# Kernel tuning notes

Measured on AMD Instinct MI355X. Metric: run time of the kernel, lower is better.

The kernel has to match this reference:

```python
import jax, jax.numpy as jnp
import numpy as np

BN_EPS = 1e-5


def _bn_train(x, gamma, beta):
    # torch BatchNorm1d in training mode: normalize with batch mean and
    # biased batch variance.
    mu = jnp.mean(x, axis=0)
    var = jnp.var(x, axis=0)
    return (x - mu) * jax.lax.rsqrt(var + BN_EPS) * gamma + beta


def setup_inputs() -> dict:
    key = jax.random.key(0)
    ks = jax.random.split(key, 12)
    N, F_D, F_C, E, VOCAB, H = 16384, 26, 10, 16, 200000, 400
    D_IN = (F_D + F_C) * E  # 576
    return {
        "Xi_dense": jax.random.normal(ks[0], (N, F_D, 1), jnp.float32),
        "Xv": jax.random.uniform(ks[1], (N, F_D + F_C), jnp.float32),
        "Wd": jax.random.normal(ks[2], (F_D, E), jnp.float32) * 0.1,
        "bd": jax.random.normal(ks[3], (F_D, E), jnp.float32) * 0.1,
        "tables": jax.random.normal(ks[4], (F_C, VOCAB, E), jnp.float32) * 0.1,
        "W1": jax.random.normal(ks[5], (H, D_IN), jnp.float32) * 0.05,
        "b1": jax.random.normal(ks[6], (H,), jnp.float32) * 0.05,
        "g1": jnp.ones((H,), jnp.float32),
        "be1": jnp.zeros((H,), jnp.float32),
        "W2": jax.random.normal(ks[7], (H, H), jnp.float32) * 0.05,
        "b2": jax.random.normal(ks[8], (H,), jnp.float32) * 0.05,
        "g2": jnp.ones((H,), jnp.float32),
        "be2": jnp.zeros((H,), jnp.float32),
        "bias_vec": jax.random.normal(ks[9], (N,), jnp.float32),
        "Xi_cat": jax.random.randint(ks[10], (N, F_C, 1), 0, VOCAB, jnp.int32),
    }


def reference(Xi_dense, Xv, Wd, bd, tables, W1, b1, g1, be1,
              W2, b2, g2, be2, bias_vec, Xi_cat):
    N = Xi_dense.shape[0]
    # dense fields: per-field Linear(1, E) -> x * W + b, shape (N, 26, E)
    dense_emb = Xi_dense * Wd[None] + bd[None]  # (N,26,1)*(1,26,E) broadcast
    # categorical fields: per-field embedding lookup, shape (N, 10, E)
    cat_emb = jax.vmap(lambda tbl, idx: tbl[idx], in_axes=(0, 1), out_axes=1)(
        tables, Xi_cat[:, :, 0])
    # scale each field embedding by its Xv value
    all_emb = jnp.concatenate([dense_emb, cat_emb], axis=1) * Xv[:, :, None]  # (N,36,E)

    # fm first order: concat of all scaled field embeddings
    fm_first = all_emb.reshape(N, -1)  # (N, 576)
    # fm second order: 0.5 * ((sum)^2 - sum of squares)
    s = jnp.sum(all_emb, axis=1)                       # (N, E)
    fm_second = 0.5 * (s * s - jnp.sum(all_emb * all_emb, axis=1))  # (N, E)

    # deep part: Linear -> BatchNorm (train-mode stats) per hidden layer;
    # dropout p=0 -> identity.
    deep = fm_first
    deep = _bn_train(deep @ W1.T + b1, g1, be1)
    deep = _bn_train(deep @ W2.T + b2, g2, be2)

    total = (jnp.sum(fm_first, axis=1) + jnp.sum(fm_second, axis=1)
             + jnp.sum(deep, axis=1) + bias_vec)
    return total
```

## Files before the change

kernel.cpp:

```cpp
#include <hip/hip_runtime.h>

#define BN_EPS 1e-5f

typedef unsigned short u16;
typedef __attribute__((ext_vector_type(8))) short bf16x8;
typedef __attribute__((ext_vector_type(4))) float f32x4;

__device__ __forceinline__ u16 f2bf(float x) {
  union { float f; unsigned int u; } v; v.f = x;
  unsigned int r = v.u + 0x7fffu + ((v.u >> 16) & 1u);
  return (u16)(r >> 16);
}
__device__ __forceinline__ float bf2f(u16 h) {
  union { unsigned int u; float f; } v; v.u = ((unsigned int)h) << 16;
  return v.f;
}

__device__ __forceinline__ float wave_reduce_sum(float v) {
#pragma unroll
  for (int off = 1; off < 64; off <<= 1) v += __shfl_xor(v, off, 64);
  return v;
}

__device__ __forceinline__ void gload_lds16(const void* g, void* l) {
  __builtin_amdgcn_global_load_lds(
      (const __attribute__((address_space(1))) void*)g,
      (__attribute__((address_space(3))) void*)l, 16, 0, 0);
}

__global__ __launch_bounds__(256) void embed_prep(
    const float* __restrict__ Xi_dense, const float* __restrict__ Xv,
    const float* __restrict__ Wd, const float* __restrict__ bd,
    const float* __restrict__ tables, const int* __restrict__ Xi_cat,
    const float* __restrict__ bias_vec, const float* __restrict__ W1,
    u16* __restrict__ fm_first, float* __restrict__ partial,
    u16* __restrict__ W1h, float* __restrict__ statz) {
  const int t = threadIdx.x;
  if (blockIdx.x >= 256) {
    const int bb = blockIdx.x - 256;
    if (bb == 0) {
#pragma unroll
      for (int i = 0; i < 8; ++i) statz[i * 256 + t] = 0.f;
    }
    const int base = bb * 4096;
#pragma unroll
    for (int e = 0; e < 16; ++e) {
      const int idx = base + e * 256 + t;
      const int r = idx / 576;
      const int j = idx - r * 576;
      W1h[idx] = (r < 400) ? f2bf(W1[r * 576 + j]) : (u16)0;
    }
    return;
  }

  __shared__ float Xvs[64 * 37];
  __shared__ float Xds[64 * 27];
  __shared__ int Cis[64 * 11];
  __shared__ float Wds[416], Bds[416];
  const int n0 = blockIdx.x * 64;

  for (int i = t; i < 2304; i += 256) {
    const int r = i / 36;
    Xvs[r * 37 + (i - r * 36)] = Xv[n0 * 36 + i];
  }
  for (int i = t; i < 1664; i += 256) {
    const int r = i / 26;
    Xds[r * 27 + (i - r * 26)] = Xi_dense[n0 * 26 + i];
  }
  for (int i = t; i < 640; i += 256) {
    const int r = i / 10;
    Cis[r * 11 + (i - r * 10)] = Xi_cat[n0 * 10 + i];
  }
  for (int i = t; i < 416; i += 256) {
    Wds[i] = Wd[i];
    Bds[i] = bd[i];
  }
  __syncthreads();

  const int r = t >> 2, q = t & 3;
  const int n = n0 + r;
  const int fpar = q >> 1, eh = (q & 1) * 8;
  float s8[8] = {}, q8[8] = {};
  float sum_all = 0.f;
  u16* frow = fm_first + (size_t)n * 576;

#pragma unroll
  for (int k = 0; k < 18; ++k) {
    const int f = fpar + 2 * k;
    const float xvv = Xvs[r * 37 + f];
    float val[8];
    if (k < 13) {
      const float xd = Xds[r * 27 + f];
      const float4 w0 = *(const float4*)&Wds[f * 16 + eh];
      const float4 w1 = *(const float4*)&Wds[f * 16 + eh + 4];
      const float4 b0 = *(const float4*)&Bds[f * 16 + eh];
      const float4 b1 = *(const float4*)&Bds[f * 16 + eh + 4];
      val[0] = fmaf(xd, w0.x, b0.x) * xvv;
      val[1] = fmaf(xd, w0.y, b0.y) * xvv;
      val[2] = fmaf(xd, w0.z, b0.z) * xvv;
      val[3] = fmaf(xd, w0.w, b0.w) * xvv;
      val[4] = fmaf(xd, w1.x, b1.x) * xvv;
      val[5] = fmaf(xd, w1.y, b1.y) * xvv;
      val[6] = fmaf(xd, w1.z, b1.z) * xvv;
      val[7] = fmaf(xd, w1.w, b1.w) * xvv;
    } else {
      const int fc = f - 26;
      const int row = Cis[r * 11 + fc];
      const float* tp =
          tables + ((size_t)fc * 200000 + (size_t)row) * 16 + eh;
      const float4 v0 = *(const float4*)tp;
      const float4 v1 = *(const float4*)(tp + 4);
      val[0] = v0.x * xvv;
      val[1] = v0.y * xvv;
      val[2] = v0.z * xvv;
      val[3] = v0.w * xvv;
      val[4] = v1.x * xvv;
      val[5] = v1.y * xvv;
      val[6] = v1.z * xvv;
      val[7] = v1.w * xvv;
    }
    bf16x8 o;
#pragma unroll
    for (int j = 0; j < 8; ++j) {
      s8[j] += val[j];
      q8[j] += val[j] * val[j];
      sum_all += val[j];
      o[j] = (short)f2bf(val[j]);
    }
    *(bf16x8*)&frow[f * 16 + eh] = o;
  }

  float fm2h = 0.f;
#pragma unroll
  for (int j = 0; j < 8; ++j) {
    const float se = s8[j] + __shfl_xor(s8[j], 2, 64);
    const float qe = q8[j] + __shfl_xor(q8[j], 2, 64);
    fm2h += se * se - qe;
  }
  const float fm2 = 0.5f * (fm2h + __shfl_xor(fm2h, 1, 64));
  float srow = sum_all + __shfl_xor(sum_all, 1, 64);
  srow += __shfl_xor(srow, 2, 64);
  if (q == 0) partial[n] = srow + fm2 + bias_vec[n];
}

template <int NFR>
__device__ __forceinline__ void gemm_body(
    const u16* __restrict__ A, int lda, const u16* __restrict__ W, int ldw,
    const float* __restrict__ bias, int nbias, u16* __restrict__ Y, int ldc,
    int Ncap, float* __restrict__ aS, float* __restrict__ aQ, int K,
    int bx, int by, u16* As, u16* Bs, float (&rS)[2][4][2][16],
    float (&rQ)[2][4][2][16]) {
  const int t = threadIdx.x;
  const int bm = bx * 64;
  const int bn = by * 128;
  const int wid = t >> 6, lane = t & 63;
  const int wr = wid >> 1, wc = wid & 1;
  const int lr = lane & 15, lk = (lane >> 4) * 8;
  const int sr = lane >> 2;
  const int sk = (lane & 3) * 8;
  const bool active = (NFR == 4) || (wc == 0);

  f32x4 acc[2][NFR] = {};

  for (int kt = 0; kt < K; kt += 32) {
    gload_lds16(&A[(size_t)(bm + wid * 16 + sr) * lda + kt + sk],
                &As[wid * 512]);
#pragma unroll
    for (int i = 0; i < 2; ++i) {
      const int c = wid * 2 + i;
      if (NFR == 4 || c < 2)
        gload_lds16(&W[(size_t)(bn + c * 16 + sr) * ldw + kt + sk],
                    &Bs[c * 512]);
    }
    __syncthreads();

    if (active) {
      bf16x8 af[2], bfv[NFR];
#pragma unroll
      for (int mf = 0; mf < 2; ++mf)
        af[mf] = *(const bf16x8*)&As[(wr * 32 + mf * 16 + lr) * 32 + lk];
#pragma unroll
      for (int nf = 0; nf < NFR; ++nf)
        bfv[nf] = *(const bf16x8*)&Bs[(wc * 64 + nf * 16 + lr) * 32 + lk];
#pragma unroll
      for (int mf = 0; mf < 2; ++mf)
#pragma unroll
        for (int nf = 0; nf < NFR; ++nf)
          acc[mf][nf] = __builtin_amdgcn_mfma_f32_16x16x32_bf16(
              af[mf], bfv[nf], acc[mf][nf], 0, 0, 0);
    }
    __syncthreads();
  }

  const int l4 = (lane >> 4) * 4;
  if (active) {
#pragma unroll
    for (int nf = 0; nf < NFR; ++nf) {
      const int col = bn + wc * 64 + nf * 16 + lr;
      const float bb = (col < nbias) ? bias[col] : 0.f;
      float s = 0.f, q = 0.f;
#pragma unroll
      for (int mf = 0; mf < 2; ++mf) {
#pragma unroll
        for (int r = 0; r < 4; ++r) {
          const int row = bm + wr * 32 + mf * 16 + l4 + r;
          const float v = acc[mf][nf][r] + bb;
          s += v;
          q += v * v;
          if (col < Ncap) Y[(size_t)row * ldc + col] = f2bf(v);
        }
      }
      s += __shfl_xor(s, 16, 64);
      s += __shfl_xor(s, 32, 64);
      q += __shfl_xor(q, 16, 64);
      q += __shfl_xor(q, 32, 64);
      if (lane < 16) {
        rS[wc][nf][wr][lr] = s;
        rQ[wc][nf][wr][lr] = q;
      }
    }
  }
  __syncthreads();
  if (t < (NFR == 4 ? 128 : 32)) {
    const int wcc = t >> 6, nff = (t >> 4) & 3, c = t & 15;
    atomicAdd(&aS[bn + t], rS[wcc][nff][0][c] + rS[wcc][nff][1][c]);
    atomicAdd(&aQ[bn + t], rQ[wcc][nff][0][c] + rQ[wcc][nff][1][c]);
  }
}

__global__ __launch_bounds__(256) void gemm_bf16(
    const u16* __restrict__ A, int lda,
    const u16* __restrict__ W, int ldw,
    const float* __restrict__ bias, int nbias,
    u16* __restrict__ Y, int ldc, int Ncap,
    float* __restrict__ aS, float* __restrict__ aQ, int K) {
  __shared__ u16 As[64 * 32];
  __shared__ u16 Bs[128 * 32];
  __shared__ float rS[2][4][2][16];
  __shared__ float rQ[2][4][2][16];
  const int bid = blockIdx.x;
  const int l = (bid & 7) * (gridDim.x >> 3) + (bid >> 3);
  const int bx = l >> 2, by = l & 3;
  if (by < 3)
    gemm_body<4>(A, lda, W, ldw, bias, nbias, Y, ldc, Ncap, aS, aQ, K,
                 bx, by, As, Bs, rS, rQ);
  else
    gemm_body<2>(A, lda, W, ldw, bias, nbias, Y, ldc, Ncap, aS, aQ, K,
                 bx, by, As, Bs, rS, rQ);
}

__device__ __forceinline__ void bn_affine4(const float* aS, const float* aQ,
                                           const float* g, const float* be,
                                           int j, float4& aa, float4& cc) {
  const float4 S = *(const float4*)&aS[j];
  const float4 Q = *(const float4*)&aQ[j];
  const float4 G = *(const float4*)&g[j];
  const float4 E = *(const float4*)&be[j];
  const float inv = 1.f / 16384.f;
  float mu, var;
  mu = S.x * inv; var = Q.x * inv - mu * mu;
  aa.x = G.x * rsqrtf(var + BN_EPS); cc.x = E.x - mu * aa.x;
  mu = S.y * inv; var = Q.y * inv - mu * mu;
  aa.y = G.y * rsqrtf(var + BN_EPS); cc.y = E.y - mu * aa.y;
  mu = S.z * inv; var = Q.z * inv - mu * mu;
  aa.z = G.z * rsqrtf(var + BN_EPS); cc.z = E.z - mu * aa.z;
  mu = S.w * inv; var = Q.w * inv - mu * mu;
  aa.w = G.w * rsqrtf(var + BN_EPS); cc.w = E.w - mu * aa.w;
}

__global__ __launch_bounds__(256) void prep2(
    const float* __restrict__ aS1, const float* __restrict__ aQ1,
    const float* __restrict__ g1, const float* __restrict__ be1,
    const float* __restrict__ W2, const float* __restrict__ b2,
    u16* __restrict__ W2p, float* __restrict__ b2p) {
  const int t = threadIdx.x;
  const int lane = t & 63;
  const int row = blockIdx.x * 4 + (t >> 6);
  const ushort4 z4 = {0, 0, 0, 0};
  if (row >= 400) {
    const int j1 = lane * 4;
    *(ushort4*)&W2p[(size_t)row * 416 + j1] = z4;
    const int j2 = 256 + lane * 4;
    if (j2 < 416) *(ushort4*)&W2p[(size_t)row * 416 + j2] = z4;
    if (lane == 0) b2p[row] = 0.f;
    return;
  }
  float dot = 0.f;
  {
    const int j = lane * 4;
    float4 aa, cc;
    bn_affine4(aS1, aQ1, g1, be1, j, aa, cc);
    const float4 w = *(const float4*)&W2[(size_t)row * 400 + j];
    ushort4 o = {f2bf(w.x * aa.x), f2bf(w.y * aa.y), f2bf(w.z * aa.z),
                 f2bf(w.w * aa.w)};
    *(ushort4*)&W2p[(size_t)row * 416 + j] = o;
    dot += w.x * cc.x + w.y * cc.y + w.z * cc.z + w.w * cc.w;
  }
  {
    const int j = 256 + lane * 4;
    if (j < 400) {
      float4 aa, cc;
      bn_affine4(aS1, aQ1, g1, be1, j, aa, cc);
      const float4 w = *(const float4*)&W2[(size_t)row * 400 + j];
      ushort4 o = {f2bf(w.x * aa.x), f2bf(w.y * aa.y), f2bf(w.z * aa.z),
                   f2bf(w.w * aa.w)};
      *(ushort4*)&W2p[(size_t)row * 416 + j] = o;
      dot += w.x * cc.x + w.y * cc.y + w.z * cc.z + w.w * cc.w;
    } else if (j < 416) {
      *(ushort4*)&W2p[(size_t)row * 416 + j] = z4;
    }
  }
  dot = wave_reduce_sum(dot);
  if (lane == 0) b2p[row] = b2[row] + dot;
}

__global__ __launch_bounds__(256) void final_kernel(
    const u16* __restrict__ Y2, const float* __restrict__ aS2,
    const float* __restrict__ aQ2, const float* __restrict__ g2,
    const float* __restrict__ be2, const float* __restrict__ partial,
    float* __restrict__ out) {
  const int t = threadIdx.x;
  const int lane = t & 63;
  const int wid = t >> 6;
  const int j0 = lane * 8;
  float ar[8], cr[8];
  if (j0 < 400) {
    float4 aa0, cc0, aa1, cc1;
    bn_affine4(aS2, aQ2, g2, be2, j0, aa0, cc0);
    bn_affine4(aS2, aQ2, g2, be2, j0 + 4, aa1, cc1);
    ar[0] = aa0.x; ar[1] = aa0.y; ar[2] = aa0.z; ar[3] = aa0.w;
    ar[4] = aa1.x; ar[5] = aa1.y; ar[6] = aa1.z; ar[7] = aa1.w;
    cr[0] = cc0.x; cr[1] = cc0.y; cr[2] = cc0.z; cr[3] = cc0.w;
    cr[4] = cc1.x; cr[5] = cc1.y; cr[6] = cc1.z; cr[7] = cc1.w;
  } else {
#pragma unroll
    for (int k = 0; k < 8; ++k) { ar[k] = 0.f; cr[k] = 0.f; }
  }
#pragma unroll
  for (int r = 0; r < 4; ++r) {
    const int n = blockIdx.x * 16 + wid * 4 + r;
    float acc = 0.f;
    if (j0 < 400) {
      const bf16x8 y = *(const bf16x8*)&Y2[(size_t)n * 400 + j0];
#pragma unroll
      for (int k = 0; k < 8; ++k)
        acc += fmaf(ar[k], bf2f((u16)y[k]), cr[k]);
    }
    acc = wave_reduce_sum(acc);
    if (lane == 0) out[n] = partial[n] + acc;
  }
}

extern "C" void kernel_launch(void* const* d_in, const int* in_sizes, int n_in,
                              void* d_out, int out_size, void* d_ws,
                              size_t ws_size, hipStream_t stream) {
  const float* Xi_dense = (const float*)d_in[0];
  const float* Xv = (const float*)d_in[1];
  const float* Wd = (const float*)d_in[2];
  const float* bd = (const float*)d_in[3];
  const float* tables = (const float*)d_in[4];
  const float* W1 = (const float*)d_in[5];
  const float* b1 = (const float*)d_in[6];
  const float* g1 = (const float*)d_in[7];
  const float* be1 = (const float*)d_in[8];
  const float* W2 = (const float*)d_in[9];
  const float* b2 = (const float*)d_in[10];
  const float* g2 = (const float*)d_in[11];
  const float* be2 = (const float*)d_in[12];
  const float* bias_vec = (const float*)d_in[13];
  const int* Xi_cat = (const int*)d_in[14];

  constexpr int N = 16384;
  constexpr int DIN = 576;
  constexpr int H = 400;
  constexpr int KP = 416;
  constexpr int WPAD = 512;
  constexpr int NXB = 256;

  u16* fm_first = (u16*)d_ws;
  u16* Y1h = fm_first + (size_t)N * DIN;
  u16* Y2h = Y1h + (size_t)N * KP;
  u16* W1h = Y2h + (size_t)N * H;
  u16* W2p = W1h + (size_t)WPAD * DIN;
  float* fptr = (float*)(W2p + (size_t)WPAD * KP);
  float* partial = fptr;
  float* aS1 = partial + N;
  float* aQ1 = aS1 + WPAD;
  float* aS2 = aQ1 + WPAD;
  float* aQ2 = aS2 + WPAD;
  float* b2p = aQ2 + WPAD;

  embed_prep<<<256 + 72, 256, 0, stream>>>(Xi_dense, Xv, Wd, bd, tables,
                                           Xi_cat, bias_vec, W1, fm_first,
                                           partial, W1h, aS1);

  gemm_bf16<<<NXB * 4, 256, 0, stream>>>(fm_first, DIN, W1h, DIN, b1, H,
                                         Y1h, KP, KP, aS1, aQ1, DIN);

  prep2<<<128, 256, 0, stream>>>(aS1, aQ1, g1, be1, W2, b2, W2p, b2p);

  gemm_bf16<<<NXB * 4, 256, 0, stream>>>(Y1h, KP, W2p, KP, b2p, H,
                                         Y2h, H, H, aS2, aQ2, KP);

  final_kernel<<<N / 16, 256, 0, stream>>>(Y2h, aS2, aQ2, g2, be2, partial,
                                           (float*)d_out);
}
```

Measured before the change: 69.79 us.

## Drop linear biases cancelled by train-mode BatchNorm and widen embed parallelism

Train-mode BatchNorm subtracts the batch mean, so any per-column constant added before it cancels. The change therefore removes the b1/b2 bias adds from the GEMM epilogues and drops the folded-bias dot product (and beta1) from prep2, which becomes a simple elementwise weight-scaling kernel. Separately, embed_prep now handles 32 rows per block with 8 threads per row instead of 64 rows with 4 threads, doubling the block count and adding one extra shuffle stage to the reductions. This relies on the algebraic cancellation being exact; bf16 rounding of the unbiased activations changes slightly.

```diff
diff --git a/kernel.cpp b/kernel.cpp
--- a/kernel.cpp
+++ b/kernel.cpp
@@ -36,8 +36,8 @@
     u16* __restrict__ fm_first, float* __restrict__ partial,
     u16* __restrict__ W1h, float* __restrict__ statz) {
   const int t = threadIdx.x;
-  if (blockIdx.x >= 256) {
-    const int bb = blockIdx.x - 256;
+  if (blockIdx.x >= 512) {
+    const int bb = blockIdx.x - 512;
     if (bb == 0) {
 #pragma unroll
       for (int i = 0; i < 8; ++i) statz[i * 256 + t] = 0.f;
@@ -53,21 +53,21 @@
     return;
   }
 
-  __shared__ float Xvs[64 * 37];
-  __shared__ float Xds[64 * 27];
-  __shared__ int Cis[64 * 11];
+  __shared__ float Xvs[32 * 37];
+  __shared__ float Xds[32 * 27];
+  __shared__ int Cis[32 * 11];
   __shared__ float Wds[416], Bds[416];
-  const int n0 = blockIdx.x * 64;
-
-  for (int i = t; i < 2304; i += 256) {
+  const int n0 = blockIdx.x * 32;
+
+  for (int i = t; i < 1152; i += 256) {
     const int r = i / 36;
     Xvs[r * 37 + (i - r * 36)] = Xv[n0 * 36 + i];
   }
-  for (int i = t; i < 1664; i += 256) {
+  for (int i = t; i < 832; i += 256) {
     const int r = i / 26;
     Xds[r * 27 + (i - r * 26)] = Xi_dense[n0 * 26 + i];
   }
-  for (int i = t; i < 640; i += 256) {
+  for (int i = t; i < 320; i += 256) {
     const int r = i / 10;
     Cis[r * 11 + (i - r * 10)] = Xi_cat[n0 * 10 + i];
   }
@@ -77,32 +77,32 @@
   }
   __syncthreads();
 
-  const int r = t >> 2, q = t & 3;
+  const int r = t >> 3, q = t & 7;
   const int n = n0 + r;
-  const int fpar = q >> 1, eh = (q & 1) * 8;
+  const int fbase = q >> 1, eh = (q & 1) * 8;
   float s8[8] = {}, q8[8] = {};
   float sum_all = 0.f;
   u16* frow = fm_first + (size_t)n * 576;
 
 #pragma unroll
-  for (int k = 0; k < 18; ++k) {
-    const int f = fpar + 2 * k;
+  for (int j = 0; j < 9; ++j) {
+    const int f = fbase + 4 * j;
     const float xvv = Xvs[r * 37 + f];
     float val[8];
-    if (k < 13) {
+    if (f < 26) {
       const float xd = Xds[r * 27 + f];
       const float4 w0 = *(const float4*)&Wds[f * 16 + eh];
       const float4 w1 = *(const float4*)&Wds[f * 16 + eh + 4];
       const float4 b0 = *(const float4*)&Bds[f * 16 + eh];
-      const float4 b1 = *(const float4*)&Bds[f * 16 + eh + 4];
+      const float4 b1v = *(const float4*)&Bds[f * 16 + eh + 4];
       val[0] = fmaf(xd, w0.x, b0.x) * xvv;
       val[1] = fmaf(xd, w0.y, b0.y) * xvv;
       val[2] = fmaf(xd, w0.z, b0.z) * xvv;
       val[3] = fmaf(xd, w0.w, b0.w) * xvv;
-      val[4] = fmaf(xd, w1.x, b1.x) * xvv;
-      val[5] = fmaf(xd, w1.y, b1.y) * xvv;
-      val[6] = fmaf(xd, w1.z, b1.z) * xvv;
-      val[7] = fmaf(xd, w1.w, b1.w) * xvv;
+      val[4] = fmaf(xd, w1.x, b1v.x) * xvv;
+      val[5] = fmaf(xd, w1.y, b1v.y) * xvv;
+      val[6] = fmaf(xd, w1.z, b1v.z) * xvv;
+      val[7] = fmaf(xd, w1.w, b1v.w) * xvv;
     } else {
       const int fc = f - 26;
       const int row = Cis[r * 11 + fc];
@@ -121,35 +121,37 @@
     }
     bf16x8 o;
 #pragma unroll
-    for (int j = 0; j < 8; ++j) {
-      s8[j] += val[j];
-      q8[j] += val[j] * val[j];
-      sum_all += val[j];
-      o[j] = (short)f2bf(val[j]);
+    for (int jj = 0; jj < 8; ++jj) {
+      s8[jj] += val[jj];
+      q8[jj] += val[jj] * val[jj];
+      sum_all += val[jj];
+      o[jj] = (short)f2bf(val[jj]);
     }
     *(bf16x8*)&frow[f * 16 + eh] = o;
   }
 
   float fm2h = 0.f;
 #pragma unroll
-  for (int j = 0; j < 8; ++j) {
-    const float se = s8[j] + __shfl_xor(s8[j], 2, 64);
-    const float qe = q8[j] + __shfl_xor(q8[j], 2, 64);
+  for (int jj = 0; jj < 8; ++jj) {
+    float se = s8[jj] + __shfl_xor(s8[jj], 2, 64);
+    se += __shfl_xor(se, 4, 64);
+    float qe = q8[jj] + __shfl_xor(q8[jj], 2, 64);
+    qe += __shfl_xor(qe, 4, 64);
     fm2h += se * se - qe;
   }
   const float fm2 = 0.5f * (fm2h + __shfl_xor(fm2h, 1, 64));
   float srow = sum_all + __shfl_xor(sum_all, 1, 64);
   srow += __shfl_xor(srow, 2, 64);
+  srow += __shfl_xor(srow, 4, 64);
   if (q == 0) partial[n] = srow + fm2 + bias_vec[n];
 }
 
 template <int NFR>
 __device__ __forceinline__ void gemm_body(
     const u16* __restrict__ A, int lda, const u16* __restrict__ W, int ldw,
-    const float* __restrict__ bias, int nbias, u16* __restrict__ Y, int ldc,
-    int Ncap, float* __restrict__ aS, float* __restrict__ aQ, int K,
-    int bx, int by, u16* As, u16* Bs, float (&rS)[2][4][2][16],
-    float (&rQ)[2][4][2][16]) {
+    u16* __restrict__ Y, int ldc, int Ncap, float* __restrict__ aS,
+    float* __restrict__ aQ, int K, int bx, int by, u16* As, u16* Bs,
+    float (&rS)[2][4][2][16], float (&rQ)[2][4][2][16]) {
   const int t = threadIdx.x;
   const int bm = bx * 64;
   const int bn = by * 128;
@@ -197,14 +199,13 @@
 #pragma unroll
     for (int nf = 0; nf < NFR; ++nf) {
       const int col = bn + wc * 64 + nf * 16 + lr;
-      const float bb = (col < nbias) ? bias[col] : 0.f;
       float s = 0.f, q = 0.f;
 #pragma unroll
       for (int mf = 0; mf < 2; ++mf) {
 #pragma unroll
         for (int r = 0; r < 4; ++r) {
           const int row = bm + wr * 32 + mf * 16 + l4 + r;
-          const float v = acc[mf][nf][r] + bb;
+          const float v = acc[mf][nf][r];
           s += v;
           q += v * v;
           if (col < Ncap) Y[(size_t)row * ldc + col] = f2bf(v);
@@ -231,7 +232,6 @@
 __global__ __launch_bounds__(256) void gemm_bf16(
     const u16* __restrict__ A, int lda,
     const u16* __restrict__ W, int ldw,
-    const float* __restrict__ bias, int nbias,
     u16* __restrict__ Y, int ldc, int Ncap,
     float* __restrict__ aS, float* __restrict__ aQ, int K) {
   __shared__ u16 As[64 * 32];
@@ -242,11 +242,38 @@
   const int l = (bid & 7) * (gridDim.x >> 3) + (bid >> 3);
   const int bx = l >> 2, by = l & 3;
   if (by < 3)
-    gemm_body<4>(A, lda, W, ldw, bias, nbias, Y, ldc, Ncap, aS, aQ, K,
-                 bx, by, As, Bs, rS, rQ);
+    gemm_body<4>(A, lda, W, ldw, Y, ldc, Ncap, aS, aQ, K, bx, by, As, Bs,
+                 rS, rQ);
   else
-    gemm_body<2>(A, lda, W, ldw, bias, nbias, Y, ldc, Ncap, aS, aQ, K,
-                 bx, by, As, Bs, rS, rQ);
+    gemm_body<2>(A, lda, W, ldw, Y, ldc, Ncap, aS, aQ, K, bx, by, As, Bs,
+                 rS, rQ);
+}
+
+__global__ __launch_bounds__(256) void prep2(
+    const float* __restrict__ aS1, const float* __restrict__ aQ1,
+    const float* __restrict__ g1, const float* __restrict__ W2,
+    u16* __restrict__ W2p) {
+  const int c = blockIdx.x * 256 + threadIdx.x;
+  const int row = c / 104;
+  const int jc = (c - row * 104) * 4;
+  ushort4 o = {0, 0, 0, 0};
+  if (row < 400 && jc < 400) {
+    const float4 S = *(const float4*)&aS1[jc];
+    const float4 Q = *(const float4*)&aQ1[jc];
+    const float4 G = *(const float4*)&g1[jc];
+    const float4 w = *(const float4*)&W2[(size_t)row * 400 + jc];
+    const float inv = 1.f / 16384.f;
+    float mu, var, a;
+    mu = S.x * inv; var = Q.x * inv - mu * mu;
+    a = G.x * rsqrtf(var + BN_EPS); o.x = f2bf(w.x * a);
+    mu = S.y * inv; var = Q.y * inv - mu * mu;
+    a = G.y * rsqrtf(var + BN_EPS); o.y = f2bf(w.y * a);
+    mu = S.z * inv; var = Q.z * inv - mu * mu;
+    a = G.z * rsqrtf(var + BN_EPS); o.z = f2bf(w.z * a);
+    mu = S.w * inv; var = Q.w * inv - mu * mu;
+    a = G.w * rsqrtf(var + BN_EPS); o.w = f2bf(w.w * a);
+  }
+  *(ushort4*)&W2p[(size_t)row * 416 + jc] = o;
 }
 
 __device__ __forceinline__ void bn_affine4(const float* aS, const float* aQ,
@@ -266,52 +293,6 @@
   aa.z = G.z * rsqrtf(var + BN_EPS); cc.z = E.z - mu * aa.z;
   mu = S.w * inv; var = Q.w * inv - mu * mu;
   aa.w = G.w * rsqrtf(var + BN_EPS); cc.w = E.w - mu * aa.w;
-}
-
-__global__ __launch_bounds__(256) void prep2(
-    const float* __restrict__ aS1, const float* __restrict__ aQ1,
-    const float* __restrict__ g1, const float* __restrict__ be1,
-    const float* __restrict__ W2, const float* __restrict__ b2,
-    u16* __restrict__ W2p, float* __restrict__ b2p) {
-  const int t = threadIdx.x;
-  const int lane = t & 63;
-  const int row = blockIdx.x * 4 + (t >> 6);
-  const ushort4 z4 = {0, 0, 0, 0};
-  if (row >= 400) {
-    const int j1 = lane * 4;
-    *(ushort4*)&W2p[(size_t)row * 416 + j1] = z4;
-    const int j2 = 256 + lane * 4;
-    if (j2 < 416) *(ushort4*)&W2p[(size_t)row * 416 + j2] = z4;
-    if (lane == 0) b2p[row] = 0.f;
-    return;
-  }
-  float dot = 0.f;
-  {
-    const int j = lane * 4;
-    float4 aa, cc;
-    bn_affine4(aS1, aQ1, g1, be1, j, aa, cc);
-    const float4 w = *(const float4*)&W2[(size_t)row * 400 + j];
-    ushort4 o = {f2bf(w.x * aa.x), f2bf(w.y * aa.y), f2bf(w.z * aa.z),
-                 f2bf(w.w * aa.w)};
-    *(ushort4*)&W2p[(size_t)row * 416 + j] = o;
-    dot += w.x * cc.x + w.y * cc.y + w.z * cc.z + w.w * cc.w;
-  }
-  {
-    const int j = 256 + lane * 4;
-    if (j < 400) {
-      float4 aa, cc;
-      bn_affine4(aS1, aQ1, g1, be1, j, aa, cc);
-      const float4 w = *(const float4*)&W2[(size_t)row * 400 + j];
-      ushort4 o = {f2bf(w.x * aa.x), f2bf(w.y * aa.y), f2bf(w.z * aa.z),
-                   f2bf(w.w * aa.w)};
-      *(ushort4*)&W2p[(size_t)row * 416 + j] = o;
-      dot += w.x * cc.x + w.y * cc.y + w.z * cc.z + w.w * cc.w;
-    } else if (j < 416) {
-      *(ushort4*)&W2p[(size_t)row * 416 + j] = z4;
-    }
-  }
-  dot = wave_reduce_sum(dot);
-  if (lane == 0) b2p[row] = b2[row] + dot;
 }
 
 __global__ __launch_bounds__(256) void final_kernel(
@@ -360,11 +341,8 @@
   const float* bd = (const float*)d_in[3];
   const float* tables = (const float*)d_in[4];
   const float* W1 = (const float*)d_in[5];
-  const float* b1 = (const float*)d_in[6];
   const float* g1 = (const float*)d_in[7];
-  const float* be1 = (const float*)d_in[8];
   const float* W2 = (const float*)d_in[9];
-  const float* b2 = (const float*)d_in[10];
   const float* g2 = (const float*)d_in[11];
   const float* be2 = (const float*)d_in[12];
   const float* bias_vec = (const float*)d_in[13];
@@ -388,18 +366,17 @@
   float* aQ1 = aS1 + WPAD;
   float* aS2 = aQ1 + WPAD;
   float* aQ2 = aS2 + WPAD;
-  float* b2p = aQ2 + WPAD;
-
-  embed_prep<<<256 + 72, 256, 0, stream>>>(Xi_dense, Xv, Wd, bd, tables,
+
+  embed_prep<<<512 + 72, 256, 0, stream>>>(Xi_dense, Xv, Wd, bd, tables,
                                            Xi_cat, bias_vec, W1, fm_first,
                                            partial, W1h, aS1);
 
-  gemm_bf16<<<NXB * 4, 256, 0, stream>>>(fm_first, DIN, W1h, DIN, b1, H,
+  gemm_bf16<<<NXB * 4, 256, 0, stream>>>(fm_first, DIN, W1h, DIN,
                                          Y1h, KP, KP, aS1, aQ1, DIN);
 
-  prep2<<<128, 256, 0, stream>>>(aS1, aQ1, g1, be1, W2, b2, W2p, b2p);
-
-  gemm_bf16<<<NXB * 4, 256, 0, stream>>>(Y1h, KP, W2p, KP, b2p, H,
+  prep2<<<208, 256, 0, stream>>>(aS1, aQ1, g1, W2, W2p);
+
+  gemm_bf16<<<NXB * 4, 256, 0, stream>>>(Y1h, KP, W2p, KP,
                                          Y2h, H, H, aS2, aQ2, KP);
 
   final_kernel<<<N / 16, 256, 0, stream>>>(Y2h, aS2, aQ2, g2, be2, partial,
```

Measured after the change: 65.27 us. 6.5% less time.
